# Kernel optimization log

Measured on AMD Instinct MI355X. Metric: run time of the kernel, lower is better.

Reference implementation:

```python
import jax, jax.numpy as jnp
import numpy as np

B, L, CH, NH, NB = 32, 512, 512, 8, 2
HD = CH // NH
NEG = -4294967295.0  # -2**32 + 1, as in the torch code


def _ln(x, g, b, eps=1e-8):
    m = x.mean(-1, keepdims=True)
    v = ((x - m) ** 2).mean(-1, keepdims=True)
    return (x - m) / jnp.sqrt(v + eps) * g + b


def _forward(log_seqs, seqs_nxt, t, qw, qb, kw, kb, vw, vb,
             ln1g, ln1b, ln2g, ln2b, c1w, c1b, c2w, c2b,
             posK, posV, lng, lnb, tw0, tb0, tw1, tb1, tw2, tb2,
             decw, decb):
    # causal mask (mode='training'): True = masked (~tril)
    mask = jnp.triu(jnp.ones((L, L), dtype=bool), k=1)
    pK = posK[:L].reshape(L, NH, HD)  # shared relative/absolute pos per head
    pV = posV[:L].reshape(L, NH, HD)
    seqs = log_seqs
    for i in range(NB):
        Qin = _ln(seqs, ln1g[i], ln1b[i])
        # note: Q from layernormed input, K/V from raw seqs (as in torch code)
        Q = (Qin @ qw[i].T + qb[i]).reshape(B, L, NH, HD)
        K = (seqs @ kw[i].T + kb[i]).reshape(B, L, NH, HD)
        V = (seqs @ vw[i].T + vb[i]).reshape(B, L, NH, HD)
        scores = jnp.einsum('blhd,bmhd->bhlm', Q, K)
        scores = scores + jnp.einsum('blhd,mhd->bhlm', Q, pK)
        scores = scores / jnp.sqrt(jnp.float32(HD))
        scores = jnp.where(mask, NEG, scores)
        w = jax.nn.softmax(scores, axis=-1)
        out = jnp.einsum('bhlm,bmhd->blhd', w, V) + jnp.einsum('bhlm,mhd->blhd', w, pV)
        seqs = Qin + out.reshape(B, L, CH)  # residual from layernormed Q
        seqs = _ln(seqs, ln2g[i], ln2b[i])
        # PointWiseFeedForward: conv1d kernel_size=1 == linear; residual inside
        h = jax.nn.relu(seqs @ c1w[i].T + c1b[i])
        seqs = seqs + (h @ c2w[i].T + c2b[i])
    log_feats = _ln(seqs, lng, lnb)

    # diffusion timestep embedding
    half = CH // 2
    freqs = jnp.exp(jnp.arange(half, dtype=jnp.float32) * (-np.log(10000.0) / (half - 1)))
    ang = t.astype(jnp.float32)[:, None] * freqs[None, :]
    temb = jnp.concatenate([jnp.sin(ang), jnp.cos(ang)], axis=1)  # [B, CH]
    temb = temb @ tw0.T + tb0
    temb = temb * jax.nn.sigmoid(temb)  # swish nonlinearity
    temb = temb @ tw1.T + tb1
    temb = temb * jax.nn.sigmoid(temb)
    temb = temb @ tw2.T + tb2
    x_t = seqs_nxt + temb[:, None, :]

    # non-conditional decoder path: decoder(cat([log_feats, x_t], -1))
    dec = jnp.concatenate([log_feats, x_t], axis=-1) @ decw.T + decb
    return (log_feats, dec)


def setup_inputs() -> dict:
    key = jax.random.key(0)
    ks = jax.random.split(key, 24)
    s = 0.02

    def n(k, shape):
        return jax.random.normal(k, shape, jnp.float32) * s

    return {
        'log_seqs': jax.random.normal(ks[0], (B, L, CH), jnp.float32),
        'seqs_nxt': jax.random.normal(ks[1], (B, L, CH), jnp.float32),
        't': jax.random.randint(ks[2], (B,), 0, 1000, jnp.int32),
        'qw': n(ks[3], (NB, CH, CH)), 'qb': jnp.zeros((NB, CH), jnp.float32),
        'kw': n(ks[4], (NB, CH, CH)), 'kb': jnp.zeros((NB, CH), jnp.float32),
        'vw': n(ks[5], (NB, CH, CH)), 'vb': jnp.zeros((NB, CH), jnp.float32),
        'ln1g': jnp.ones((NB, CH), jnp.float32), 'ln1b': jnp.zeros((NB, CH), jnp.float32),
        'ln2g': jnp.ones((NB, CH), jnp.float32), 'ln2b': jnp.zeros((NB, CH), jnp.float32),
        'c1w': n(ks[6], (NB, CH, CH)), 'c1b': jnp.zeros((NB, CH), jnp.float32),
        'c2w': n(ks[7], (NB, CH, CH)), 'c2b': jnp.zeros((NB, CH), jnp.float32),
        'posK': n(ks[8], (L, CH)), 'posV': n(ks[9], (L, CH)),
        'lng': jnp.ones((CH,), jnp.float32), 'lnb': jnp.zeros((CH,), jnp.float32),
        'tw0': n(ks[10], (4 * CH, CH)), 'tb0': jnp.zeros((4 * CH,), jnp.float32),
        'tw1': n(ks[11], (4 * CH, 4 * CH)), 'tb1': jnp.zeros((4 * CH,), jnp.float32),
        'tw2': n(ks[12], (CH, 4 * CH)), 'tb2': jnp.zeros((CH,), jnp.float32),
        'decw': n(ks[13], (CH, 2 * CH)), 'decb': jnp.zeros((CH,), jnp.float32),
    }


def reference(log_seqs, seqs_nxt, t, qw, qb, kw, kb, vw, vb,
              ln1g, ln1b, ln2g, ln2b, c1w, c1b, c2w, c2b,
              posK, posV, lng, lnb, tw0, tb0, tw1, tb1, tw2, tb2,
              decw, decb):
    return _forward(log_seqs, seqs_nxt, t, qw, qb, kw, kb, vw, vb,
                    ln1g, ln1b, ln2g, ln2b, c1w, c1b, c2w, c2b,
                    posK, posV, lng, lnb, tw0, tb0, tw1, tb1, tw2, tb2,
                    decw, decb)
```

## Files before the change

### kernel.cpp

```cpp
#include <hip/hip_runtime.h>
#include <math.h>

#define BB 32
#define LL 512
#define CHN 512
#define NHH 8
#define HDD 64

typedef __attribute__((ext_vector_type(8))) short short8;
typedef __attribute__((ext_vector_type(4))) float f32x4;

__device__ __forceinline__ float b2f(unsigned short s) {
    union { unsigned int u; float f; } c; c.u = ((unsigned int)s) << 16; return c.f;
}
__device__ __forceinline__ unsigned short f2b(float f) {
    union { float f; unsigned int u; } c; c.f = f;
    return (unsigned short)((c.u + 0x7fffu + ((c.u >> 16) & 1u)) >> 16);
}

#define SWZ(row, col) ((((row) * 64 + (col))) ^ (((row) & 7) << 3))

__device__ __forceinline__ void gl16(const unsigned short* g, unsigned short* l) {
    __builtin_amdgcn_global_load_lds(
        (const __attribute__((address_space(1))) unsigned int*)g,
        (__attribute__((address_space(3))) unsigned int*)l, 16, 0, 0);
}

__global__ __launch_bounds__(256) void cvt_kernel(
    const float* __restrict__ x, unsigned short* __restrict__ y, int n4)
{
    int i = blockIdx.x * 256 + threadIdx.x;
    if (i >= n4) return;
    const float4 v = reinterpret_cast<const float4*>(x)[i];
    ushort4 o;
    o.x = f2b(v.x); o.y = f2b(v.y); o.z = f2b(v.z); o.w = f2b(v.w);
    reinterpret_cast<ushort4*>(y)[i] = o;
}

__global__ __launch_bounds__(256) void cvt6_kernel(
    const float* __restrict__ p0, const float* __restrict__ p1,
    const float* __restrict__ p2, const float* __restrict__ p3,
    const float* __restrict__ p4, const float* __restrict__ p5,
    unsigned short* __restrict__ y)
{
    const int j = blockIdx.y;
    const float* x = j == 0 ? p0 : j == 1 ? p1 : j == 2 ? p2
                   : j == 3 ? p3 : j == 4 ? p4 : p5;
    const int i = blockIdx.x * 256 + threadIdx.x;
    const float4 v = reinterpret_cast<const float4*>(x)[i];
    ushort4 o;
    o.x = f2b(v.x); o.y = f2b(v.y); o.z = f2b(v.z); o.w = f2b(v.w);
    reinterpret_cast<ushort4*>(y + (size_t)j * 524288)[i] = o;
}

__global__ __launch_bounds__(256) void ln_kernel(
    const float* __restrict__ x, const float* __restrict__ g,
    const float* __restrict__ b, float* __restrict__ yf,
    unsigned short* __restrict__ yb)
{
    const int row = blockIdx.x;
    const int tid = threadIdx.x;
    const size_t base = (size_t)row * CHN;
    float2 v = *reinterpret_cast<const float2*>(x + base + tid * 2);
    float s  = v.x + v.y;
    float ss = v.x * v.x + v.y * v.y;
    #pragma unroll
    for (int m = 1; m < 64; m <<= 1) {
        s  += __shfl_xor(s, m);
        ss += __shfl_xor(ss, m);
    }
    __shared__ float red[8];
    const int wave = tid >> 6;
    if ((tid & 63) == 0) { red[wave] = s; red[4 + wave] = ss; }
    __syncthreads();
    s  = red[0] + red[1] + red[2] + red[3];
    ss = red[4] + red[5] + red[6] + red[7];
    const float mean = s * (1.0f / CHN);
    const float var  = ss * (1.0f / CHN) - mean * mean;
    const float inv  = rsqrtf(var + 1e-8f);
    const int c = tid * 2;
    float2 o;
    o.x = (v.x - mean) * inv * g[c]     + b[c];
    o.y = (v.y - mean) * inv * g[c + 1] + b[c + 1];
    if (yf) *reinterpret_cast<float2*>(yf + base + c) = o;
    if (yb) {
        ushort2 ob; ob.x = f2b(o.x); ob.y = f2b(o.y);
        *reinterpret_cast<ushort2*>(yb + base + c) = ob;
    }
}

template <int NT>
__device__ __forceinline__ void gemm_body(
    const unsigned short* __restrict__ A,
    const unsigned short* __restrict__ A2,
    const unsigned short* __restrict__ W, int ldw,
    const float* __restrict__ bias,
    const float* __restrict__ pos,
    const float* __restrict__ res,
    float* __restrict__ outf,
    unsigned short* __restrict__ outb,
    unsigned short* __restrict__ outbt,
    int act, int bid)
{
    __shared__ alignas(16) unsigned short lA[3][8192];
    __shared__ alignas(16) unsigned short lB[3][4096];

    const int tid  = threadIdx.x;
    const int lane = tid & 63;
    const int wid  = tid >> 6;

    const int swz = (bid & 7) * 32 + (bid >> 3);
    const int by = swz >> 2, bx = swz & 3;
    const int bm = by * 256, bn = bx * 128;

    const int ia0 = wid * 2, ia1 = wid * 2 + 1;
    const int hiA0 = ia0 >> 2, rgA0 = ia0 & 3;
    const int hiA1 = ia1 >> 2, rgA1 = ia1 & 3;
    const int hiB = wid >> 1, rgB = wid & 1;

    const unsigned short* Ax = A2 ? A2 : A;
    const unsigned short* aS0  = A  + (size_t)(bm + rgA0 * 64 + lane) * 512 + hiA0 * 8;
    const unsigned short* aS1  = A  + (size_t)(bm + rgA1 * 64 + lane) * 512 + hiA1 * 8;
    const unsigned short* a2S0 = Ax + (size_t)(bm + rgA0 * 64 + lane) * 512 + hiA0 * 8;
    const unsigned short* a2S1 = Ax + (size_t)(bm + rgA1 * 64 + lane) * 512 + hiA1 * 8;
    const unsigned short* wS   = W + (size_t)(bn + rgB * 64 + lane) * ldw + hiB * 8;
    const int dA0 = (hiA0 * 256 + rgA0 * 64) * 8;
    const int dA1 = (hiA1 * 256 + rgA1 * 64) * 8;
    const int dB  = (hiB * 128 + rgB * 64) * 8;

    const int wr = wid >> 1, wc = wid & 1;
    const int fr = lane & 15;
    const int fq = lane >> 4;

    f32x4 acc[4][4];
    #pragma unroll
    for (int m = 0; m < 4; ++m)
        #pragma unroll
        for (int n = 0; n < 4; ++n)
            acc[m][n] = (f32x4){0.f, 0.f, 0.f, 0.f};

    #define MG_STAGE(buf, t)                                            \
        do {                                                            \
            const int k0 = ((t) & 15) * 32;                             \
            const unsigned short* s0 = ((t) < 16) ? aS0 : a2S0;         \
            const unsigned short* s1 = ((t) < 16) ? aS1 : a2S1;         \
            gl16(s0 + k0, &lA[buf][dA0]);                               \
            gl16(s1 + k0, &lA[buf][dA1]);                               \
            gl16(wS + (t) * 32, &lB[buf][dB]);                          \
        } while (0)

    MG_STAGE(0, 0);
    MG_STAGE(1, 1);

    #pragma unroll
    for (int t = 0; t < NT; ++t) {
        const int cur = t % 3;
        if (t + 2 < NT) {
            MG_STAGE((t + 2) % 3, t + 2);
            asm volatile("s_waitcnt vmcnt(6)" ::: "memory");
        } else if (t + 1 < NT) {
            asm volatile("s_waitcnt vmcnt(3)" ::: "memory");
        } else {
            asm volatile("s_waitcnt vmcnt(0)" ::: "memory");
        }
        __builtin_amdgcn_s_barrier();

        const unsigned short* pa = &lA[cur][(fq * 256 + wr * 64 + fr) * 8];
        const unsigned short* pb = &lB[cur][(fq * 128 + wc * 64 + fr) * 8];
        short8 aF[4], bF[4];
        #pragma unroll
        for (int m = 0; m < 4; ++m)
            aF[m] = *reinterpret_cast<const short8*>(pa + m * 128);
        #pragma unroll
        for (int n = 0; n < 4; ++n)
            bF[n] = *reinterpret_cast<const short8*>(pb + n * 128);
        asm volatile("s_waitcnt lgkmcnt(0)" ::: "memory");
        __builtin_amdgcn_s_barrier();

        __builtin_amdgcn_s_setprio(1);
        #pragma unroll
        for (int m = 0; m < 4; ++m)
            #pragma unroll
            for (int n = 0; n < 4; ++n)
                acc[m][n] = __builtin_amdgcn_mfma_f32_16x16x32_bf16(
                    aF[m], bF[n], acc[m][n], 0, 0, 0);
        __builtin_amdgcn_s_setprio(0);
    }
    #undef MG_STAGE

    const int row0 = bm + wr * 64, col0 = bn + wc * 64;
    #pragma unroll
    for (int m = 0; m < 4; ++m) {
        #pragma unroll
        for (int n = 0; n < 4; ++n) {
            const int col = col0 + n * 16 + fr;
            const float bia = bias ? bias[col] : 0.f;
            ushort4 o4;
            #pragma unroll
            for (int r = 0; r < 4; ++r) {
                const int row = row0 + m * 16 + fq * 4 + r;
                float v = acc[m][n][r] + bia;
                if (pos) v += pos[(size_t)(row & (LL - 1)) * CHN + col];
                if (act == 1) v = fmaxf(v, 0.f);
                const size_t idx = (size_t)row * CHN + col;
                if (res) v += res[idx];
                if (outf) outf[idx] = v;
                if (outb) outb[idx] = f2b(v);
                ((unsigned short*)&o4)[r] = f2b(v);
            }
            if (outbt) {
                const int rw = row0 + m * 16 + fq * 4;
                *reinterpret_cast<ushort4*>(
                    &outbt[((size_t)(rw >> 9) * 512 + col) * 512 + (rw & 511)]) = o4;
            }
        }
    }
}

__global__ __launch_bounds__(512) void mgemm_kernel(
    const unsigned short* __restrict__ A,
    const unsigned short* __restrict__ W, int ldw,
    const float* __restrict__ bias,
    const float* __restrict__ pos,
    const float* __restrict__ res,
    float* __restrict__ outf,
    unsigned short* __restrict__ outb,
    unsigned short* __restrict__ outbt,
    int act)
{
    gemm_body<16>(A, nullptr, W, ldw, bias, pos, res, outf, outb, outbt, act,
                  blockIdx.x);
}

__global__ __launch_bounds__(512) void qkv_kernel(
    const unsigned short* __restrict__ qinb, const unsigned short* __restrict__ curb,
    const unsigned short* __restrict__ Wq, const unsigned short* __restrict__ Wk,
    const unsigned short* __restrict__ Wv,
    const float* __restrict__ qb, const float* __restrict__ kb,
    const float* __restrict__ vb,
    const float* __restrict__ posK, const float* __restrict__ posV,
    unsigned short* __restrict__ QBb, unsigned short* __restrict__ KBb,
    unsigned short* __restrict__ VTb)
{
    const int job = blockIdx.y;
    const unsigned short* A = (job == 0) ? qinb : curb;
    const unsigned short* W = (job == 0) ? Wq : (job == 1) ? Wk : Wv;
    const float* bias = (job == 0) ? qb : (job == 1) ? kb : vb;
    const float* pos  = (job == 0) ? nullptr : (job == 1) ? posK : posV;
    unsigned short* outb  = (job == 0) ? QBb : (job == 1) ? KBb : nullptr;
    unsigned short* outbt = (job == 2) ? VTb : nullptr;
    gemm_body<16>(A, nullptr, W, 512, bias, pos, nullptr, nullptr, outb, outbt, 0,
                  blockIdx.x);
}

__global__ __launch_bounds__(512) void dec_kernel(
    const unsigned short* __restrict__ R0b, const unsigned short* __restrict__ R1b,
    const unsigned short* __restrict__ Wd, const float* __restrict__ decb,
    float* __restrict__ dec)
{
    gemm_body<32>(R0b, R1b, Wd, 1024, decb, nullptr, nullptr, dec, nullptr, nullptr,
                  0, blockIdx.x);
}

__global__ __launch_bounds__(256) void skgemm_kernel(
    const float* __restrict__ A, int K,
    const float* __restrict__ W, int N,
    float* __restrict__ P)
{
    __shared__ float As[32][128];
    const int tid = threadIdx.x;
    const int kz  = blockIdx.y;
    const int c   = blockIdx.x * 256 + tid;

    #pragma unroll
    for (int i = 0; i < 16; ++i) {
        const int idx = i * 256 + tid;
        const int r = idx >> 7, k = idx & 127;
        As[r][k] = A[(size_t)r * K + kz * 128 + k];
    }
    __syncthreads();

    float acc[32];
    #pragma unroll
    for (int r = 0; r < 32; ++r) acc[r] = 0.f;

    const float* wrow = W + (size_t)c * K + kz * 128;
    for (int k4 = 0; k4 < 32; ++k4) {
        const float4 w = reinterpret_cast<const float4*>(wrow)[k4];
        #pragma unroll
        for (int r = 0; r < 32; ++r) {
            const float4 a = *reinterpret_cast<const float4*>(&As[r][k4 * 4]);
            acc[r] = fmaf(w.x, a.x, fmaf(w.y, a.y, fmaf(w.z, a.z, fmaf(w.w, a.w, acc[r]))));
        }
    }

    float* pp = P + ((size_t)kz * N + c) * 32;
    #pragma unroll
    for (int r = 0; r < 32; ++r) pp[r] = acc[r];
}

__global__ __launch_bounds__(256) void skreduce_kernel(
    const float* __restrict__ P, int KS, const float* __restrict__ bias,
    float* __restrict__ out, int N, int act)
{
    const int idx = blockIdx.x * 256 + threadIdx.x;
    const int r = idx & 31, c = idx >> 5;
    float s = 0.f;
    for (int kz = 0; kz < KS; ++kz)
        s += P[(size_t)kz * N * 32 + idx];
    s += bias[c];
    if (act == 2) s = s / (1.f + __expf(-s));
    out[(size_t)r * N + c] = s;
}

__global__ __launch_bounds__(256) void mattn_kernel(
    const unsigned short* __restrict__ Q, const unsigned short* __restrict__ K,
    const unsigned short* __restrict__ VT, const unsigned short* __restrict__ Qin,
    float* __restrict__ Sout)
{
    __shared__ alignas(16) unsigned short kT[2][4096];
    __shared__ alignas(16) unsigned short vT[2][4096];
    __shared__ unsigned short pl[4][1024];

    const int qt = blockIdx.x;
    const int h  = blockIdx.y;
    const int b  = blockIdx.z;
    const int tid = threadIdx.x, lane = tid & 63, wid = tid >> 6;
    const int fr = lane & 15, fq = lane >> 4;
    const int hc = h * HDD;

    const int c0i = tid, c1i = 256 + tid;
    const int r0s = c0i >> 3, j0s = c0i & 7, d0s = ((j0s ^ (r0s & 7)) << 3);
    const int r1s = c1i >> 3, j1s = c1i & 7, d1s = ((j1s ^ (r1s & 7)) << 3);
    const unsigned short* kS0 = K + (size_t)b * LL * CHN + (size_t)r0s * CHN + hc + d0s;
    const unsigned short* kS1 = K + (size_t)b * LL * CHN + (size_t)r1s * CHN + hc + d1s;
    const unsigned short* vS0 = VT + ((size_t)(b * NHH + h) * 64 + r0s) * 512 + d0s;
    const unsigned short* vS1 = VT + ((size_t)(b * NHH + h) * 64 + r1s) * 512 + d1s;

    #define AT_STAGE(buf, ch)                                              \
        do {                                                               \
            const int o = (ch) * 64;                                       \
            gl16(kS0 + (size_t)o * CHN, &kT[buf][wid * 512]);              \
            gl16(kS1 + (size_t)o * CHN, &kT[buf][2048 + wid * 512]);       \
            gl16(vS0 + o, &vT[buf][wid * 512]);                            \
            gl16(vS1 + o, &vT[buf][2048 + wid * 512]);                     \
        } while (0)

    const size_t qrow = (size_t)b * LL + qt * 64 + wid * 16 + fr;
    short8 qf[2];
    qf[0] = *reinterpret_cast<const short8*>(Q + qrow * CHN + hc + fq * 8);
    qf[1] = *reinterpret_cast<const short8*>(Q + qrow * CHN + hc + 32 + fq * 8);

    f32x4 oacc[4];
    #pragma unroll
    for (int n = 0; n < 4; ++n) oacc[n] = (f32x4){0.f, 0.f, 0.f, 0.f};
    float mrow[4], lrow[4];
    #pragma unroll
    for (int r = 0; r < 4; ++r) { mrow[r] = -1e30f; lrow[r] = 0.f; }

    AT_STAGE(0, 0);
    __syncthreads();

    for (int ch = 0; ch <= qt; ++ch) {
        const int cur = ch & 1;
        if (ch < qt) AT_STAGE(cur ^ 1, ch + 1);

        f32x4 sacc[4];
        #pragma unroll
        for (int n = 0; n < 4; ++n) sacc[n] = (f32x4){0.f, 0.f, 0.f, 0.f};
        __builtin_amdgcn_s_setprio(1);
        #pragma unroll
        for (int kk = 0; kk < 2; ++kk) {
            #pragma unroll
            for (int n = 0; n < 4; ++n) {
                const short8 kf = *reinterpret_cast<const short8*>(
                    &kT[cur][SWZ(n * 16 + fr, kk * 32 + fq * 8)]);
                sacc[n] = __builtin_amdgcn_mfma_f32_16x16x32_bf16(qf[kk], kf, sacc[n], 0, 0, 0);
            }
        }
        __builtin_amdgcn_s_setprio(0);

        const bool diag = (ch == qt);
        #pragma unroll
        for (int r = 0; r < 4; ++r) {
            float sv[4];
            #pragma unroll
            for (int n = 0; n < 4; ++n) {
                float v = sacc[n][r] * 0.125f;
                if (diag && (n * 16 + fr > wid * 16 + fq * 4 + r)) v = -1e30f;
                sv[n] = v;
            }
            float cm = fmaxf(fmaxf(sv[0], sv[1]), fmaxf(sv[2], sv[3]));
            cm = fmaxf(cm, __shfl_xor(cm, 1));
            cm = fmaxf(cm, __shfl_xor(cm, 2));
            cm = fmaxf(cm, __shfl_xor(cm, 4));
            cm = fmaxf(cm, __shfl_xor(cm, 8));
            const float mn = fmaxf(mrow[r], cm);
            const float f = __expf(mrow[r] - mn);
            mrow[r] = mn;
            float ps = 0.f;
            #pragma unroll
            for (int n = 0; n < 4; ++n) { sv[n] = __expf(sv[n] - mn); ps += sv[n]; }
            ps += __shfl_xor(ps, 1);
            ps += __shfl_xor(ps, 2);
            ps += __shfl_xor(ps, 4);
            ps += __shfl_xor(ps, 8);
            lrow[r] = lrow[r] * f + ps;
            #pragma unroll
            for (int n = 0; n < 4; ++n) {
                oacc[n][r] *= f;
                pl[wid][SWZ(fq * 4 + r, n * 16 + fr)] = f2b(sv[n]);
            }
        }

        __builtin_amdgcn_s_setprio(1);
        #pragma unroll
        for (int kk = 0; kk < 2; ++kk) {
            const short8 pa = *reinterpret_cast<const short8*>(
                &pl[wid][SWZ(fr, kk * 32 + fq * 8)]);
            #pragma unroll
            for (int n = 0; n < 4; ++n) {
                const short8 vf = *reinterpret_cast<const short8*>(
                    &vT[cur][SWZ(n * 16 + fr, kk * 32 + fq * 8)]);
                oacc[n] = __builtin_amdgcn_mfma_f32_16x16x32_bf16(pa, vf, oacc[n], 0, 0, 0);
            }
        }
        __builtin_amdgcn_s_setprio(0);
        __syncthreads();
    }
    #undef AT_STAGE

    const size_t orow0 = (size_t)b * LL + qt * 64 + wid * 16 + fq * 4;
    #pragma unroll
    for (int r = 0; r < 4; ++r) {
        const float inv = 1.f / lrow[r];
        const size_t rowidx = (orow0 + r) * CHN + hc;
        #pragma unroll
        for (int n = 0; n < 4; ++n) {
            const int d = n * 16 + fr;
            Sout[rowidx + d] = oacc[n][r] * inv + b2f(Qin[rowidx + d]);
        }
    }
}

__global__ __launch_bounds__(256) void temb_embed_kernel(
    const int* __restrict__ t, float* __restrict__ T0)
{
    const int idx = blockIdx.x * 256 + threadIdx.x;
    const int b = idx >> 9, j = idx & 511;
    const float tv = (float)t[b];
    const int jj = (j < 256) ? j : j - 256;
    const float freq = __expf((float)jj * (-9.210340371976184f / 255.f));
    const float ang = tv * freq;
    T0[idx] = (j < 256) ? sinf(ang) : cosf(ang);
}

__global__ __launch_bounds__(256) void add_temb_kernel(
    const float* __restrict__ xin, const float* __restrict__ temb,
    unsigned short* __restrict__ out)
{
    const size_t i4 = (size_t)blockIdx.x * 256 + threadIdx.x;
    const size_t elem = i4 * 4;
    const int b = (int)(elem >> 18);
    const int c = (int)(elem & (CHN - 1));
    const float4 a = reinterpret_cast<const float4*>(xin)[i4];
    const float4 tv = *reinterpret_cast<const float4*>(temb + (size_t)b * CHN + c);
    ushort4 o;
    o.x = f2b(a.x + tv.x); o.y = f2b(a.y + tv.y);
    o.z = f2b(a.z + tv.z); o.w = f2b(a.w + tv.w);
    reinterpret_cast<ushort4*>(out)[i4] = o;
}

extern "C" void kernel_launch(void* const* d_in, const int* in_sizes, int n_in,
                              void* d_out, int out_size, void* d_ws, size_t ws_size,
                              hipStream_t stream)
{
    (void)in_sizes; (void)n_in; (void)out_size; (void)ws_size;
    const float* log_seqs = (const float*)d_in[0];
    const float* seqs_nxt = (const float*)d_in[1];
    const int*   tt       = (const int*)d_in[2];
    const float* qw  = (const float*)d_in[3];
    const float* qb  = (const float*)d_in[4];
    const float* kw  = (const float*)d_in[5];
    const float* kb  = (const float*)d_in[6];
    const float* vw  = (const float*)d_in[7];
    const float* vb  = (const float*)d_in[8];
    const float* ln1g = (const float*)d_in[9];
    const float* ln1b = (const float*)d_in[10];
    const float* ln2g = (const float*)d_in[11];
    const float* ln2b = (const float*)d_in[12];
    const float* c1w = (const float*)d_in[13];
    const float* c1b = (const float*)d_in[14];
    const float* c2w = (const float*)d_in[15];
    const float* c2b = (const float*)d_in[16];
    const float* posK = (const float*)d_in[17];
    const float* posV = (const float*)d_in[18];
    const float* lng = (const float*)d_in[19];
    const float* lnb = (const float*)d_in[20];
    const float* tw0 = (const float*)d_in[21];
    const float* tb0 = (const float*)d_in[22];
    const float* tw1 = (const float*)d_in[23];
    const float* tb1 = (const float*)d_in[24];
    const float* tw2 = (const float*)d_in[25];
    const float* tb2 = (const float*)d_in[26];
    const float* decw = (const float*)d_in[27];
    const float* decb = (const float*)d_in[28];

    const size_t SZ = (size_t)BB * LL * CHN;
    const int M = BB * LL;
    float* out = (float*)d_out;
    float* log_feats = out;
    float* dec = out + SZ;
    unsigned short* QBb = (unsigned short*)dec;
    unsigned short* VTb = (unsigned short*)log_feats;

    float* ws = (float*)d_ws;
    float* S = ws;
    unsigned short* KBb = (unsigned short*)(ws + SZ);
    unsigned short* R0  = (unsigned short*)(ws + SZ + SZ / 2);
    unsigned short* R1  = (unsigned short*)(ws + 2 * SZ);
    unsigned short* WBu = (unsigned short*)(ws + 2 * SZ + SZ / 2);
    float* T0 = ws + 2 * SZ + SZ / 2 + 1572864;
    float* T1 = T0 + 32 * CHN;
    float* T2 = T1 + 32 * 2048;
    float* T3 = T2 + 32 * 2048;
    float* P  = S;

    const size_t WQ = 0, WK = 524288, WV = 1048576, WC1 = 1572864,
                 WC2 = 2097152, WDEC = 2621440;

    auto mg = [&](const unsigned short* A, const unsigned short* W, int ldw,
                  const float* bias, const float* pos, const float* res,
                  float* outf, unsigned short* outb, unsigned short* outbt, int act) {
        mgemm_kernel<<<256, 512, 0, stream>>>(A, W, ldw, bias, pos, res,
                                              outf, outb, outbt, act);
    };
    auto skg = [&](const float* A, int K, const float* W, int N,
                   const float* bias, float* o, int act) {
        skgemm_kernel<<<dim3(N / 256, K / 128), 256, 0, stream>>>(A, K, W, N, P);
        skreduce_kernel<<<(N * 32) / 256, 256, 0, stream>>>(P, K / 128, bias, o, N, act);
    };

    cvt6_kernel<<<dim3(512, 6), 256, 0, stream>>>(qw, kw, vw, c1w, c2w, decw, WBu);
    cvt_kernel<<<(int)(SZ / 4 / 256), 256, 0, stream>>>(log_seqs, R1, (int)(SZ / 4));

    const float* cur = log_seqs;
    for (int i = 0; i < 2; ++i) {
        const size_t wo = (size_t)i * 262144;
        const size_t bo = (size_t)i * CHN;
        unsigned short* qinb = (i == 0) ? R0 : R1;
        unsigned short* curb = (i == 0) ? R1 : R0;
        unsigned short* smb  = qinb;
        unsigned short* hb   = curb;
        unsigned short* ncb  = (i == 0) ? qinb : nullptr;

        ln_kernel<<<M, 256, 0, stream>>>(cur, ln1g + bo, ln1b + bo, nullptr, qinb);
        qkv_kernel<<<dim3(256, 3), 512, 0, stream>>>(
            qinb, curb, WBu + WQ + wo, WBu + WK + wo, WBu + WV + wo,
            qb + bo, kb + bo, vb + bo, posK, posV, QBb, KBb, VTb);
        mattn_kernel<<<dim3(LL / 64, NHH, BB), 256, 0, stream>>>(QBb, KBb, VTb, qinb, S);
        ln_kernel<<<M, 256, 0, stream>>>(S, ln2g + bo, ln2b + bo, S, smb);
        mg(smb, WBu + WC1 + wo, 512, c1b + bo, nullptr, nullptr, nullptr, hb, nullptr, 1);
        mg(hb, WBu + WC2 + wo, 512, c2b + bo, nullptr, S, S, ncb, nullptr, 0);
        cur = S;
    }

    ln_kernel<<<M, 256, 0, stream>>>(S, lng, lnb, log_feats, R0);

    temb_embed_kernel<<<(BB * CHN) / 256, 256, 0, stream>>>(tt, T0);
    skg(T0, 512, tw0, 2048, tb0, T1, 2);
    skg(T1, 2048, tw1, 2048, tb1, T2, 2);
    skg(T2, 2048, tw2, 512, tb2, T3, 0);
    add_temb_kernel<<<(M * CHN / 4) / 256, 256, 0, stream>>>(seqs_nxt, T3, R1);

    dec_kernel<<<256, 512, 0, stream>>>(R0, R1, WBu + WDEC, decb, dec);
}
```

Measured before the change: 678.0 us.

## Pair complementary causal query tiles per attention block for load balance

```diff
diff --git a/kernel.cpp b/kernel.cpp
--- a/kernel.cpp
+++ b/kernel.cpp
@@ -322,7 +322,8 @@
     __shared__ alignas(16) unsigned short vT[2][4096];
     __shared__ unsigned short pl[4][1024];
 
-    const int qt = blockIdx.x;
+    const int pr = blockIdx.x;
+    const int qtA = pr, qtB = 7 - pr;
     const int h  = blockIdx.y;
     const int b  = blockIdx.z;
     const int tid = threadIdx.x, lane = tid & 63, wid = tid >> 6;
@@ -346,25 +347,26 @@
             gl16(vS1 + o, &vT[buf][2048 + wid * 512]);                     \
         } while (0)
 
-    const size_t qrow = (size_t)b * LL + qt * 64 + wid * 16 + fr;
-    short8 qf[2];
-    qf[0] = *reinterpret_cast<const short8*>(Q + qrow * CHN + hc + fq * 8);
-    qf[1] = *reinterpret_cast<const short8*>(Q + qrow * CHN + hc + 32 + fq * 8);
-
-    f32x4 oacc[4];
-    #pragma unroll
-    for (int n = 0; n < 4; ++n) oacc[n] = (f32x4){0.f, 0.f, 0.f, 0.f};
-    float mrow[4], lrow[4];
-    #pragma unroll
-    for (int r = 0; r < 4; ++r) { mrow[r] = -1e30f; lrow[r] = 0.f; }
-
-    AT_STAGE(0, 0);
-    __syncthreads();
-
-    for (int ch = 0; ch <= qt; ++ch) {
-        const int cur = ch & 1;
-        if (ch < qt) AT_STAGE(cur ^ 1, ch + 1);
-
+    const size_t qrowA = (size_t)b * LL + qtA * 64 + wid * 16 + fr;
+    const size_t qrowB = (size_t)b * LL + qtB * 64 + wid * 16 + fr;
+    short8 qfA[2], qfB[2];
+    qfA[0] = *reinterpret_cast<const short8*>(Q + qrowA * CHN + hc + fq * 8);
+    qfA[1] = *reinterpret_cast<const short8*>(Q + qrowA * CHN + hc + 32 + fq * 8);
+    qfB[0] = *reinterpret_cast<const short8*>(Q + qrowB * CHN + hc + fq * 8);
+    qfB[1] = *reinterpret_cast<const short8*>(Q + qrowB * CHN + hc + 32 + fq * 8);
+
+    f32x4 oaccA[4], oaccB[4];
+    float mA_[4], lA_[4], mB_[4], lB_[4];
+    #pragma unroll
+    for (int n = 0; n < 4; ++n) {
+        oaccA[n] = (f32x4){0.f, 0.f, 0.f, 0.f};
+        oaccB[n] = (f32x4){0.f, 0.f, 0.f, 0.f};
+    }
+    #pragma unroll
+    for (int r = 0; r < 4; ++r) { mA_[r] = -1e30f; lA_[r] = 0.f; mB_[r] = -1e30f; lB_[r] = 0.f; }
+
+    auto tile_step = [&](int cur, int qt, int ch, const short8* qf,
+                         f32x4* oacc, float* mrow, float* lrow) {
         f32x4 sacc[4];
         #pragma unroll
         for (int n = 0; n < 4; ++n) sacc[n] = (f32x4){0.f, 0.f, 0.f, 0.f};
@@ -426,19 +428,38 @@
             }
         }
         __builtin_amdgcn_s_setprio(0);
+    };
+
+    AT_STAGE(0, 0);
+    __syncthreads();
+
+    for (int ch = 0; ch <= qtB; ++ch) {
+        const int cur = ch & 1;
+        if (ch < qtB) AT_STAGE(cur ^ 1, ch + 1);
+
+        tile_step(cur, qtB, ch, qfB, oaccB, mB_, lB_);
+        if (ch <= qtA)
+            tile_step(cur, qtA, ch, qfA, oaccA, mA_, lA_);
+
         __syncthreads();
     }
     #undef AT_STAGE
 
-    const size_t orow0 = (size_t)b * LL + qt * 64 + wid * 16 + fq * 4;
-    #pragma unroll
-    for (int r = 0; r < 4; ++r) {
-        const float inv = 1.f / lrow[r];
-        const size_t rowidx = (orow0 + r) * CHN + hc;
-        #pragma unroll
-        for (int n = 0; n < 4; ++n) {
-            const int d = n * 16 + fr;
-            Sout[rowidx + d] = oacc[n][r] * inv + b2f(Qin[rowidx + d]);
+    #pragma unroll
+    for (int s = 0; s < 2; ++s) {
+        const int qt = s ? qtB : qtA;
+        const f32x4* oacc = s ? oaccB : oaccA;
+        const float* lrow = s ? lB_ : lA_;
+        const size_t orow0 = (size_t)b * LL + qt * 64 + wid * 16 + fq * 4;
+        #pragma unroll
+        for (int r = 0; r < 4; ++r) {
+            const float inv = 1.f / lrow[r];
+            const size_t rowidx = (orow0 + r) * CHN + hc;
+            #pragma unroll
+            for (int n = 0; n < 4; ++n) {
+                const int d = n * 16 + fr;
+                Sout[rowidx + d] = oacc[n][r] * inv + b2f(Qin[rowidx + d]);
+            }
         }
     }
 }
@@ -558,7 +579,7 @@
         qkv_kernel<<<dim3(256, 3), 512, 0, stream>>>(
             qinb, curb, WBu + WQ + wo, WBu + WK + wo, WBu + WV + wo,
             qb + bo, kb + bo, vb + bo, posK, posV, QBb, KBb, VTb);
-        mattn_kernel<<<dim3(LL / 64, NHH, BB), 256, 0, stream>>>(QBb, KBb, VTb, qinb, S);
+        mattn_kernel<<<dim3(4, NHH, BB), 256, 0, stream>>>(QBb, KBb, VTb, qinb, S);
         ln_kernel<<<M, 256, 0, stream>>>(S, ln2g + bo, ln2b + bo, S, smb);
         mg(smb, WBu + WC1 + wo, 512, c1b + bo, nullptr, nullptr, nullptr, hb, nullptr, 1);
         mg(hb, WBu + WC2 + wo, 512, c2b + bo, nullptr, S, S, ncb, nullptr, 0);
```

New measurement: 654.0 us. 1.04x faster.
